# Optimization experiments

Measured on AMD Instinct MI355X. Metric: run time of the kernel, lower is better.

## Reference

```python
import jax, jax.numpy as jnp
import numpy as np

HIDDEN = 1024
NUM_HEADS = 16
HEAD_SIZE = HIDDEN // NUM_HEADS


def setup_inputs() -> dict:
    key = jax.random.key(0)
    k1, k2, k3 = jax.random.split(key, 3)
    B, S = 2, 2048
    x = jax.random.normal(k1, (B, S, HIDDEN), dtype=jnp.float32)
    # query projection (source reuses it for both q and k)
    Wq = jax.random.normal(k2, (HIDDEN, HIDDEN), dtype=jnp.float32) / np.sqrt(HIDDEN)
    bq = jax.random.normal(k3, (HIDDEN,), dtype=jnp.float32) * 0.01
    return {"x": x, "Wq": Wq, "bq": bq}


def reference(x, Wq, bq):
    B, S, _ = x.shape
    # NOTE: source bug-for-bug: k uses the query projection too
    q = x @ Wq + bq                      # [B,S,D]
    k = x @ Wq + bq                      # [B,S,D]
    q = q.reshape(B, S, NUM_HEADS, HEAD_SIZE)
    k = k.reshape(B, S, NUM_HEADS, HEAD_SIZE)
    # scores: [B,H,S,S]
    e = jnp.einsum("bqhd,bkhd->bhqk", q, k)
    s = jax.nn.softmax(e / jnp.sqrt(jnp.float32(HEAD_SIZE)), axis=-1)
    return s
```

## Files before the change

### kernel.cpp

```cpp
#include <hip/hip_runtime.h>

#define HIDDEN 1024
#define SEQ 2048
#define NB 2
#define PSTRIDE 2052
#define NT 16

typedef _Float16 half8 __attribute__((ext_vector_type(8)));
typedef _Float16 half4 __attribute__((ext_vector_type(4)));
typedef float f32x4 __attribute__((ext_vector_type(4)));

__global__ __launch_bounds__(256) void cast_x(const float* __restrict__ x,
                                              _Float16* __restrict__ xh, int n) {
    int i = (blockIdx.x * 256 + threadIdx.x) * 4;
    if (i < n) {
        float4 v = *(const float4*)(x + i);
        half4 h;
        h[0] = (_Float16)v.x; h[1] = (_Float16)v.y;
        h[2] = (_Float16)v.z; h[3] = (_Float16)v.w;
        *(half4*)(xh + i) = h;
    }
}

__global__ __launch_bounds__(256) void cast_wt(const float* __restrict__ w,
                                               _Float16* __restrict__ wt) {
    __shared__ float tile[32][33];
    int bx = blockIdx.x * 32, by = blockIdx.y * 32;
    int tx = threadIdx.x, ty = threadIdx.y;
    #pragma unroll
    for (int i = 0; i < 32; i += 8)
        tile[ty + i][tx] = w[(by + ty + i) * HIDDEN + bx + tx];
    __syncthreads();
    #pragma unroll
    for (int i = 0; i < 32; i += 8)
        wt[(bx + ty + i) * HIDDEN + by + tx] = (_Float16)tile[tx][ty + i];
}

__global__ __launch_bounds__(256) void proj_gemm(const _Float16* __restrict__ A,
                                                 const _Float16* __restrict__ Bt,
                                                 const float* __restrict__ bias,
                                                 _Float16* __restrict__ Q) {
    __shared__ _Float16 As[128][72];
    __shared__ _Float16 Bs[128][72];
    const int m0 = blockIdx.x * 128;
    const int n0 = blockIdx.y * 128;
    const int tid = threadIdx.x;
    const int w = tid >> 6, l = tid & 63;
    const int wm = w >> 1, wn = w & 1;
    const int lrow = l & 15, lk = (l >> 4) * 8;

    f32x4 acc[4][4] = {};

    for (int k0 = 0; k0 < HIDDEN; k0 += 64) {
        __syncthreads();
        #pragma unroll
        for (int i = 0; i < 4; ++i) {
            int id = tid + i * 256;
            int r = id >> 3, c = id & 7;
            *(half8*)&As[r][c * 8] = *(const half8*)&A[(size_t)(m0 + r) * HIDDEN + k0 + c * 8];
        }
        #pragma unroll
        for (int i = 0; i < 4; ++i) {
            int id = tid + i * 256;
            int r = id >> 3, c = id & 7;
            *(half8*)&Bs[r][c * 8] = *(const half8*)&Bt[(size_t)(n0 + r) * HIDDEN + k0 + c * 8];
        }
        __syncthreads();
        #pragma unroll
        for (int kk = 0; kk < 64; kk += 32) {
            half8 af[4], bf[4];
            #pragma unroll
            for (int m = 0; m < 4; ++m)
                af[m] = *(const half8*)&As[wm * 64 + m * 16 + lrow][kk + lk];
            #pragma unroll
            for (int n = 0; n < 4; ++n)
                bf[n] = *(const half8*)&Bs[wn * 64 + n * 16 + lrow][kk + lk];
            #pragma unroll
            for (int m = 0; m < 4; ++m)
                #pragma unroll
                for (int n = 0; n < 4; ++n)
                    acc[m][n] = __builtin_amdgcn_mfma_f32_16x16x32_f16(af[m], bf[n], acc[m][n], 0, 0, 0);
        }
    }
    const int lr4 = (l >> 4) * 4, lc = l & 15;
    #pragma unroll
    for (int n = 0; n < 4; ++n) {
        int gcol = n0 + wn * 64 + n * 16 + lc;
        float b = bias[gcol];
        #pragma unroll
        for (int m = 0; m < 4; ++m) {
            #pragma unroll
            for (int r = 0; r < 4; ++r) {
                int grow = m0 + wm * 64 + m * 16 + lr4 + r;
                Q[(size_t)grow * HIDDEN + gcol] = (_Float16)(acc[m][n][r] + b);
            }
        }
    }
}

__global__ __launch_bounds__(1024, 4) void scores_softmax(const _Float16* __restrict__ Qh,
                                                          float* __restrict__ out) {
    __shared__ __align__(16) _Float16 p[2][16][PSTRIDE];
    __shared__ float rsum_lds[2][8][16];

    const int raw = blockIdx.x;
    const int xcd = raw & 7, i = raw >> 3;
    const int bh = xcd * 4 + (i >> 3);
    const int qchunk = i & 7;
    const int b = bh >> 4, h = bh & 15;

    const int tid = threadIdx.x;
    const int wv = tid >> 6;
    const int l = tid & 63;
    const int lq = l & 15, lg = l >> 4;
    const int hoff = h * 64;
    const _Float16* qbase = Qh + (size_t)b * SEQ * HIDDEN;
    const size_t outbase = (size_t)(b * 16 + h) * SEQ * SEQ;

    if (wv < 8) {
        const int pw = wv;
        const _Float16* kbase = qbase + (size_t)(pw * 256 + lq) * HIDDEN + hoff + lg * 8;
        for (int t = 0; t <= NT; ++t) {
            if (t < NT) {
                const int buf = t & 1;
                const int q0 = qchunk * 256 + t * 16;
                const _Float16* qp = qbase + (size_t)(q0 + lq) * HIDDEN + hoff + lg * 8;
                const half8 bq0 = *(const half8*)qp;
                const half8 bq1 = *(const half8*)(qp + 32);
                float rsum = 0.f;
                #pragma unroll
                for (int s = 0; s < 16; ++s) {
                    const _Float16* a = kbase + (size_t)s * 16 * HIDDEN;
                    half8 ka = *(const half8*)a;
                    half8 kb = *(const half8*)(a + 32);
                    f32x4 acc = {};
                    acc = __builtin_amdgcn_mfma_f32_16x16x32_f16(ka, bq0, acc, 0, 0, 0);
                    acc = __builtin_amdgcn_mfma_f32_16x16x32_f16(kb, bq1, acc, 0, 0, 0);
                    float e0 = exp2f(fmaf(acc[0], 0.18033688011f, -11.54156033f));
                    float e1 = exp2f(fmaf(acc[1], 0.18033688011f, -11.54156033f));
                    float e2 = exp2f(fmaf(acc[2], 0.18033688011f, -11.54156033f));
                    float e3 = exp2f(fmaf(acc[3], 0.18033688011f, -11.54156033f));
                    rsum += (e0 + e1) + (e2 + e3);
                    half4 hv;
                    hv[0] = (_Float16)e0; hv[1] = (_Float16)e1;
                    hv[2] = (_Float16)e2; hv[3] = (_Float16)e3;
                    *(half4*)&p[buf][lq][pw * 256 + s * 16 + lg * 4] = hv;
                }
                rsum += __shfl_xor(rsum, 16);
                rsum += __shfl_xor(rsum, 32);
                if (l < 16) rsum_lds[buf][pw][l] = rsum;
            }
            asm volatile("s_waitcnt lgkmcnt(0)" ::: "memory");
            __builtin_amdgcn_s_barrier();
        }
    } else {
        const int cw = wv - 8;
        for (int t = 0; t <= NT; ++t) {
            if (t > 0) {
                const int pbuf = (t - 1) & 1;
                #pragma unroll
                for (int rr = 0; rr < 2; ++rr) {
                    const int r = cw * 2 + rr;
                    float rs = 0.f;
                    #pragma unroll
                    for (int w8 = 0; w8 < 8; ++w8) rs += rsum_lds[pbuf][w8][r];
                    const float rinv = 1.0f / rs;
                    float* orow = out + outbase
                                + (size_t)(qchunk * 256 + (t - 1) * 16 + r) * SEQ;
                    #pragma unroll
                    for (int ii = 0; ii < 8; ++ii) {
                        half4 hv = *(const half4*)&p[pbuf][r][ii * 256 + l * 4];
                        f32x4 v;
                        v[0] = (float)hv[0] * rinv; v[1] = (float)hv[1] * rinv;
                        v[2] = (float)hv[2] * rinv; v[3] = (float)hv[3] * rinv;
                        __builtin_nontemporal_store(v, (f32x4*)(orow + ii * 256 + l * 4));
                    }
                }
            }
            asm volatile("s_waitcnt lgkmcnt(0)" ::: "memory");
            __builtin_amdgcn_s_barrier();
        }
    }
}

extern "C" void kernel_launch(void* const* d_in, const int* in_sizes, int n_in,
                              void* d_out, int out_size, void* d_ws, size_t ws_size,
                              hipStream_t stream) {
    const float* x  = (const float*)d_in[0];
    const float* Wq = (const float*)d_in[1];
    const float* bq = (const float*)d_in[2];
    float* out = (float*)d_out;

    _Float16* xh = (_Float16*)d_ws;
    _Float16* qh = xh + (size_t)4 * 1024 * 1024;
    _Float16* wt = qh + (size_t)4 * 1024 * 1024;

    const int nx = NB * SEQ * HIDDEN;
    cast_x<<<nx / (256 * 4), 256, 0, stream>>>(x, xh, nx);
    cast_wt<<<dim3(32, 32), dim3(32, 8), 0, stream>>>(Wq, wt);
    proj_gemm<<<dim3(NB * SEQ / 128, HIDDEN / 128), 256, 0, stream>>>(xh, wt, bq, qh);
    scores_softmax<<<256, 1024, 0, stream>>>(qh, out);
}
```

Before: 133.8 us.

## Load projection GEMM tiles directly to LDS with XOR swizzle and 512 threads

The projection GEMM now stages A and B tiles through global_load_lds direct-to-LDS copies instead of loading into registers and storing. The LDS layout uses an XOR-swizzled 16-byte slot layout in place of padded rows, to avoid bank conflicts. The block grows to 8 waves, each computing a 64x32 sub-tile, which lowers per-wave register use. The GEMM is a small share of total time next to the scores/softmax kernel, which is dominated by writing the fp32 output, so any change in overall time is likely small.

```diff
diff --git a/kernel.cpp b/kernel.cpp
--- a/kernel.cpp
+++ b/kernel.cpp
@@ -9,6 +9,10 @@
 typedef _Float16 half8 __attribute__((ext_vector_type(8)));
 typedef _Float16 half4 __attribute__((ext_vector_type(4)));
 typedef float f32x4 __attribute__((ext_vector_type(4)));
+
+#define GL2LDS(gp, lp) __builtin_amdgcn_global_load_lds( \
+    (const __attribute__((address_space(1))) void*)(gp), \
+    (__attribute__((address_space(3))) void*)(lp), 16, 0, 0)
 
 __global__ __launch_bounds__(256) void cast_x(const float* __restrict__ x,
                                               _Float16* __restrict__ xh, int n) {
@@ -36,56 +40,61 @@
         wt[(bx + ty + i) * HIDDEN + by + tx] = (_Float16)tile[tx][ty + i];
 }
 
-__global__ __launch_bounds__(256) void proj_gemm(const _Float16* __restrict__ A,
+__global__ __launch_bounds__(512) void proj_gemm(const _Float16* __restrict__ A,
                                                  const _Float16* __restrict__ Bt,
                                                  const float* __restrict__ bias,
                                                  _Float16* __restrict__ Q) {
-    __shared__ _Float16 As[128][72];
-    __shared__ _Float16 Bs[128][72];
+    __shared__ _Float16 As[128 * 64];
+    __shared__ _Float16 Bs[128 * 64];
     const int m0 = blockIdx.x * 128;
     const int n0 = blockIdx.y * 128;
     const int tid = threadIdx.x;
     const int w = tid >> 6, l = tid & 63;
-    const int wm = w >> 1, wn = w & 1;
-    const int lrow = l & 15, lk = (l >> 4) * 8;
-
-    f32x4 acc[4][4] = {};
+    const int wm = w >> 2, wn = w & 3;
+    const int lrow = l & 15, lkslot = l >> 4;
+
+    const int srow = l >> 3, sslot = l & 7;
+
+    f32x4 acc[4][2] = {};
 
     for (int k0 = 0; k0 < HIDDEN; k0 += 64) {
         __syncthreads();
         #pragma unroll
-        for (int i = 0; i < 4; ++i) {
-            int id = tid + i * 256;
-            int r = id >> 3, c = id & 7;
-            *(half8*)&As[r][c * 8] = *(const half8*)&A[(size_t)(m0 + r) * HIDDEN + k0 + c * 8];
-        }
-        #pragma unroll
-        for (int i = 0; i < 4; ++i) {
-            int id = tid + i * 256;
-            int r = id >> 3, c = id & 7;
-            *(half8*)&Bs[r][c * 8] = *(const half8*)&Bt[(size_t)(n0 + r) * HIDDEN + k0 + c * 8];
+        for (int j = 0; j < 2; ++j) {
+            const int chunk = w * 2 + j;
+            const int r = chunk * 8 + srow;
+            const int gslot = sslot ^ (r & 7);
+            GL2LDS(&A[(size_t)(m0 + r) * HIDDEN + k0 + gslot * 8], As + chunk * 512);
+            GL2LDS(&Bt[(size_t)(n0 + r) * HIDDEN + k0 + gslot * 8], Bs + chunk * 512);
         }
         __syncthreads();
         #pragma unroll
         for (int kk = 0; kk < 64; kk += 32) {
-            half8 af[4], bf[4];
-            #pragma unroll
-            for (int m = 0; m < 4; ++m)
-                af[m] = *(const half8*)&As[wm * 64 + m * 16 + lrow][kk + lk];
-            #pragma unroll
-            for (int n = 0; n < 4; ++n)
-                bf[n] = *(const half8*)&Bs[wn * 64 + n * 16 + lrow][kk + lk];
+            const int csb = kk >> 3;
+            half8 af[4], bf[2];
+            #pragma unroll
+            for (int m = 0; m < 4; ++m) {
+                const int R = wm * 64 + m * 16 + lrow;
+                const int slot = (csb + lkslot) ^ (R & 7);
+                af[m] = *(const half8*)&As[R * 64 + slot * 8];
+            }
+            #pragma unroll
+            for (int n = 0; n < 2; ++n) {
+                const int R = wn * 32 + n * 16 + lrow;
+                const int slot = (csb + lkslot) ^ (R & 7);
+                bf[n] = *(const half8*)&Bs[R * 64 + slot * 8];
+            }
             #pragma unroll
             for (int m = 0; m < 4; ++m)
                 #pragma unroll
-                for (int n = 0; n < 4; ++n)
+                for (int n = 0; n < 2; ++n)
                     acc[m][n] = __builtin_amdgcn_mfma_f32_16x16x32_f16(af[m], bf[n], acc[m][n], 0, 0, 0);
         }
     }
     const int lr4 = (l >> 4) * 4, lc = l & 15;
     #pragma unroll
-    for (int n = 0; n < 4; ++n) {
-        int gcol = n0 + wn * 64 + n * 16 + lc;
+    for (int n = 0; n < 2; ++n) {
+        int gcol = n0 + wn * 32 + n * 16 + lc;
         float b = bias[gcol];
         #pragma unroll
         for (int m = 0; m < 4; ++m) {
@@ -198,6 +207,6 @@
     const int nx = NB * SEQ * HIDDEN;
     cast_x<<<nx / (256 * 4), 256, 0, stream>>>(x, xh, nx);
     cast_wt<<<dim3(32, 32), dim3(32, 8), 0, stream>>>(Wq, wt);
-    proj_gemm<<<dim3(NB * SEQ / 128, HIDDEN / 128), 256, 0, stream>>>(xh, wt, bq, qh);
+    proj_gemm<<<dim3(NB * SEQ / 128, HIDDEN / 128), 512, 0, stream>>>(xh, wt, bq, qh);
     scores_softmax<<<256, 1024, 0, stream>>>(qh, out);
 }
```

Measured after the change: 131.4 us. No clear change (-1.8%).
